# Kernel optimization log

Hardware: AMD Instinct MI355X
Metric: run time of the kernel (lower is better)

Reference implementation:

```python
import jax, jax.numpy as jnp
import numpy as np
import math

B, NRES, RPR = 1, 384, 3
L = NRES * RPR          # 1152 rigids
CS, CZ = 256, 128
CH, H, PQ, PV = 16, 8, 8, 12


def _ln(x, scale, bias):
    mu = jnp.mean(x, axis=-1, keepdims=True)
    var = jnp.var(x, axis=-1, keepdims=True)
    return (x - mu) * jax.lax.rsqrt(var + 1e-5) * scale + bias


def _quat_to_rot(q):
    q = q / jnp.linalg.norm(q, axis=-1, keepdims=True)
    w, x, y, z = q[..., 0], q[..., 1], q[..., 2], q[..., 3]
    r = jnp.stack([
        1 - 2 * (y * y + z * z), 2 * (x * y - w * z), 2 * (x * z + w * y),
        2 * (x * y + w * z), 1 - 2 * (x * x + z * z), 2 * (y * z - w * x),
        2 * (x * z - w * y), 2 * (y * z + w * x), 1 - 2 * (x * x + y * y),
    ], axis=-1)
    return r.reshape(q.shape[:-1] + (3, 3))


def setup_inputs() -> dict:
    key = jax.random.key(0)
    ks = jax.random.split(key, 20)
    s = jax.random.normal(ks[0], (B, L, CS), jnp.float32)
    z = jax.random.normal(ks[1], (B, NRES, NRES, CZ), jnp.float32)
    rot = _quat_to_rot(jax.random.normal(ks[2], (B, L, 4), jnp.float32))
    trans = 10.0 * jax.random.normal(ks[3], (B, L, 3), jnp.float32)
    mask = jnp.ones((B, L), jnp.float32)
    rigid_to_res_idx = jnp.broadcast_to(jnp.arange(L, dtype=jnp.int32) // RPR, (B, L))
    w = lambda k, sh: 0.02 * jax.random.normal(k, sh, jnp.float32)
    return {
        "s": s, "z": z, "rot": rot, "trans": trans, "mask": mask,
        "ln_s_scale": jnp.ones((CS,), jnp.float32), "ln_s_bias": jnp.zeros((CS,), jnp.float32),
        "ln_z_scale": jnp.ones((CZ,), jnp.float32), "ln_z_bias": jnp.zeros((CZ,), jnp.float32),
        "w_q": w(ks[4], (CS, H * CH)), "w_k": w(ks[5], (CS, H * CH)), "w_v": w(ks[6], (CS, H * CH)),
        "w_qp": w(ks[7], (CS, H * PQ * 3)), "w_kp": w(ks[8], (CS, H * PQ * 3)), "w_vp": w(ks[9], (CS, H * PV * 3)),
        "w_b": w(ks[10], (CZ, H)),
        "head_weights": jnp.full((H,), 0.5413, jnp.float32),  # softplus^-1(1)
        "w_out": w(ks[11], (H * (CH + CZ + PV * 4), CS)),
        "b_out": jnp.zeros((CS,), jnp.float32),
        "rigid_to_res_idx": rigid_to_res_idx,
    }


def reference(s, z, rot, trans, mask, ln_s_scale, ln_s_bias, ln_z_scale, ln_z_bias,
              w_q, w_k, w_v, w_qp, w_kp, w_vp, w_b, head_weights, w_out, b_out,
              rigid_to_res_idx):
    b_, l_ = s.shape[0], s.shape[1]
    idx = rigid_to_res_idx[0]                       # [L] rigid -> residue, shared over batch
    s_ln = _ln(s, ln_s_scale, ln_s_bias)            # [B,L,CS]
    z_ln = _ln(z, ln_z_scale, ln_z_bias)            # [B,N,N,CZ]

    q = (s_ln @ w_q).reshape(b_, l_, H, CH)
    k = (s_ln @ w_k).reshape(b_, l_, H, CH)
    v = (s_ln @ w_v).reshape(b_, l_, H, CH)

    # local points, then rigid-transform to global frame: x_g = R x + t
    q_p = (s_ln @ w_qp).reshape(b_, l_, H, PQ, 3)
    k_p = (s_ln @ w_kp).reshape(b_, l_, H, PQ, 3)
    v_p = (s_ln @ w_vp).reshape(b_, l_, H, PV, 3)
    t5 = trans[:, :, None, None, :]
    q_g = jnp.einsum("blij,blhpj->blhpi", rot, q_p) + t5
    k_g = jnp.einsum("blij,blhpj->blhpi", rot, k_p) + t5
    v_g = jnp.einsum("blij,blhpj->blhpi", rot, v_p) + t5

    # scalar qk term
    a = jnp.einsum("blhc,bjhc->bhlj", q, k) * math.sqrt(1.0 / (3 * CH))
    # pair bias, broadcast residue-pair -> rigid-pair
    b_res = z_ln @ w_b                                # [B,N,N,H]
    b_full = b_res[:, idx][:, :, idx]                 # [B,L,L,H]
    a = a + math.sqrt(1.0 / 3) * jnp.transpose(b_full, (0, 3, 1, 2))
    # point-distance term: ||q-k||^2 = |q|^2 + |k|^2 - 2 q.k (summed over P,3)
    hw = jax.nn.softplus(head_weights) * math.sqrt(1.0 / (3 * (PQ * 9.0 / 2)))
    qq = jnp.sum(q_g * q_g, axis=(-1, -2)).transpose(0, 2, 1)   # [B,H,L]
    kk = jnp.sum(k_g * k_g, axis=(-1, -2)).transpose(0, 2, 1)
    qk = jnp.einsum("blhpc,bjhpc->bhlj", q_g, k_g)
    d2 = qq[:, :, :, None] + kk[:, :, None, :] - 2.0 * qk
    a = a - 0.5 * d2 * hw[None, :, None, None]
    a = a + (mask[:, None, None, :] - 1.0) * 1e9
    attn = jax.nn.softmax(a, axis=-1)                 # [B,H,L,L]

    o = jnp.einsum("bhlj,bjhc->blhc", attn, v)        # [B,L,H,CH]
    o_pt_g = jnp.einsum("bhlj,bjhpc->blhpc", attn, v_g)
    # back to local frame of query rigid: R^T (x - t)
    o_pt = jnp.einsum("blji,blhpj->blhpi", rot, o_pt_g - t5)
    o_pt_norm = jnp.sqrt(jnp.sum(o_pt * o_pt, axis=-1) + 1e-8)  # [B,L,H,PV]
    # pair output: sum attention over rigids belonging to each key residue
    attn_res = attn.reshape(b_, H, l_, NRES, RPR).sum(-1)       # [B,H,L,N]
    z_l = z_ln[:, idx]                                           # [B,L,N,CZ]
    o_pair = jnp.einsum("bhln,blnc->blhc", attn_res, z_l)        # [B,L,H,CZ]

    cat = jnp.concatenate(
        [o, o_pt.reshape(b_, l_, H, PV * 3), o_pt_norm, o_pair], axis=-1
    ).reshape(b_, l_, H * (CH + PV * 4 + CZ))
    return cat @ w_out + b_out                        # [B,L,CS]
```

## Files before the change

kernel.cpp:

```cpp
#include <hip/hip_runtime.h>
#include <hip/hip_bf16.h>

#define L 1152
#define NRES 384
#define CS 256
#define CZ 128
#define H 8
#define CH 16
#define PQ 8
#define PV 12
#define PSTR 1088

#define OFF_SLN  0L
#define OFF_PROJ 294912L
#define OFF_WPK  1548288L
#define OFF_QCAT 1826816L
#define OFF_KCAT 2232320L
#define OFF_VCAT 2637824L
#define OFF_BRES 3227648L
#define OFF_MURS 4407296L
#define OFF_ATTN 4702208L
#define OFF_CAT  15319040L
#define OFF_PCAT 17088512L
#define OFF_RSTAT 18268160L
#define OFF_PAV  18286592L
#define OFF_POP  21825536L

__global__ __launch_bounds__(256) void k_ln_s(const float* s, const float* sc, const float* bi, float* sln){
  int l = blockIdx.x, t = threadIdx.x;
  __shared__ float red[CS];
  float x = s[(long)l*CS + t];
  red[t] = x; __syncthreads();
  for(int st=128; st>0; st>>=1){ if(t<st) red[t]+=red[t+st]; __syncthreads(); }
  float mu = red[0] * (1.f/CS); __syncthreads();
  float d = x - mu;
  red[t] = d*d; __syncthreads();
  for(int st=128; st>0; st>>=1){ if(t<st) red[t]+=red[t+st]; __syncthreads(); }
  float var = red[0]*(1.f/CS);
  sln[(long)l*CS + t] = d*rsqrtf(var + 1e-5f)*sc[t] + bi[t];
}

__global__ __launch_bounds__(256) void k_packw(const float* wq, const float* wk, const float* wv,
                        const float* wqp, const float* wkp, const float* wvp, float* wpack){
  int k = blockIdx.x, t = threadIdx.x;
  for(int c=t; c<PSTR; c+=256){
    float v;
    if(c<128)        v = wq [(long)k*128 + c];
    else if(c<256)   v = wk [(long)k*128 + c-128];
    else if(c<384)   v = wv [(long)k*128 + c-256];
    else if(c<576)   v = wqp[(long)k*192 + c-384];
    else if(c<768)   v = wkp[(long)k*192 + c-576];
    else if(c<1056)  v = wvp[(long)k*288 + c-768];
    else             v = 0.f;
    wpack[(long)k*PSTR + c] = v;
  }
}

__global__ __launch_bounds__(256) void k_proj(const float* sln, const float* wpack, float* proj){
  int l0 = blockIdx.x*64, c0 = blockIdx.y*64, t = threadIdx.x;
  __shared__ float a_s[32][68];
  __shared__ __align__(16) float w_s[32][68];
  int tr = t>>4, tc = t&15;
  float4 acc[4] = {{0,0,0,0},{0,0,0,0},{0,0,0,0},{0,0,0,0}};
  for(int kc=0; kc<8; kc++){
    int k0 = kc*32;
    {
      int row = t>>2, kk0 = (t&3)*8;
      const float4* src = (const float4*)(sln + (long)(l0+row)*256 + k0 + kk0);
      float4 v0 = src[0], v1 = src[1];
      a_s[kk0+0][row]=v0.x; a_s[kk0+1][row]=v0.y; a_s[kk0+2][row]=v0.z; a_s[kk0+3][row]=v0.w;
      a_s[kk0+4][row]=v1.x; a_s[kk0+5][row]=v1.y; a_s[kk0+6][row]=v1.z; a_s[kk0+7][row]=v1.w;
    }
    #pragma unroll
    for(int kk2=0; kk2<2; kk2++){
      int kk = (t>>4) + 16*kk2;
      *(float4*)&w_s[kk][(t&15)*4] = *(const float4*)(wpack + (long)(k0+kk)*PSTR + c0 + (t&15)*4);
    }
    __syncthreads();
    #pragma unroll 8
    for(int kk=0; kk<32; kk++){
      float4 a4 = *(const float4*)&a_s[kk][tr*4];
      float4 b4 = *(const float4*)&w_s[kk][tc*4];
      acc[0].x+=a4.x*b4.x; acc[0].y+=a4.x*b4.y; acc[0].z+=a4.x*b4.z; acc[0].w+=a4.x*b4.w;
      acc[1].x+=a4.y*b4.x; acc[1].y+=a4.y*b4.y; acc[1].z+=a4.y*b4.z; acc[1].w+=a4.y*b4.w;
      acc[2].x+=a4.z*b4.x; acc[2].y+=a4.z*b4.y; acc[2].z+=a4.z*b4.z; acc[2].w+=a4.z*b4.w;
      acc[3].x+=a4.w*b4.x; acc[3].y+=a4.w*b4.y; acc[3].z+=a4.w*b4.z; acc[3].w+=a4.w*b4.w;
    }
    __syncthreads();
  }
  #pragma unroll
  for(int r=0;r<4;r++)
    *(float4*)(proj + (long)(l0 + tr*4 + r)*PSTR + c0 + tc*4) = acc[r];
}

__global__ __launch_bounds__(256) void k_ln_z(const float* z, const float* sc, const float* bi,
                       const float* wb, float* murs, float* bres_t){
  int t = threadIdx.x;
  long rp0 = (long)blockIdx.x*32;
  int r = t>>3, part = t&7;
  long rp = rp0 + r;
  __shared__ __align__(16) float swb[8*132];
  __shared__ float SB[8][2];
  const float4* z4 = (const float4*)z;
  float4 x0 = z4[rp*32 + part*4 + 0];
  float4 x1 = z4[rp*32 + part*4 + 1];
  float4 x2 = z4[rp*32 + part*4 + 2];
  float4 x3 = z4[rp*32 + part*4 + 3];
  #pragma unroll
  for(int k2=0;k2<4;k2++){
    int e = t + k2*256; int h = e>>7, c = e&127;
    swb[h*132 + c] = sc[c]*wb[(long)c*8 + h];
  }
  __syncthreads();
  if(t < 64){
    int h = t>>3, seg = t&7;
    float S=0, Bv=0;
    #pragma unroll
    for(int i=0;i<16;i++){
      int c = seg*16+i;
      S  += swb[h*132+c];
      Bv += bi[c]*wb[(long)c*8 + h];
    }
    #pragma unroll
    for(int off=1;off<8;off<<=1){ S += __shfl_xor(S,off,64); Bv += __shfl_xor(Bv,off,64); }
    if(seg==0){ SB[h][0]=S; SB[h][1]=Bv; }
  }
  float s1 = x0.x+x0.y+x0.z+x0.w + x1.x+x1.y+x1.z+x1.w
           + x2.x+x2.y+x2.z+x2.w + x3.x+x3.y+x3.z+x3.w;
  float s2 = x0.x*x0.x+x0.y*x0.y+x0.z*x0.z+x0.w*x0.w
           + x1.x*x1.x+x1.y*x1.y+x1.z*x1.z+x1.w*x1.w
           + x2.x*x2.x+x2.y*x2.y+x2.z*x2.z+x2.w*x2.w
           + x3.x*x3.x+x3.y*x3.y+x3.z*x3.z+x3.w*x3.w;
  #pragma unroll
  for(int off=1;off<8;off<<=1){ s1 += __shfl_xor(s1,off,64); s2 += __shfl_xor(s2,off,64); }
  float mu = s1*(1.f/CZ);
  float var = s2*(1.f/CZ) - mu*mu;
  float rstd = rsqrtf(var + 1e-5f);
  if(part==0){ murs[rp*2]=mu; murs[rp*2+1]=rstd; }
  float acc[8];
  const float4* swb4 = (const float4*)swb;
  #pragma unroll
  for(int h=0;h<8;h++){
    float4 wa = swb4[h*33 + part*4 + 0];
    float4 wbv= swb4[h*33 + part*4 + 1];
    float4 wc = swb4[h*33 + part*4 + 2];
    float4 wd = swb4[h*33 + part*4 + 3];
    acc[h] = x0.x*wa.x + x0.y*wa.y + x0.z*wa.z + x0.w*wa.w
           + x1.x*wbv.x+ x1.y*wbv.y+ x1.z*wbv.z+ x1.w*wbv.w
           + x2.x*wc.x + x2.y*wc.y + x2.z*wc.z + x2.w*wc.w
           + x3.x*wd.x + x3.y*wd.y + x3.z*wd.z + x3.w*wd.w;
  }
  #pragma unroll
  for(int off=1;off<8;off<<=1){
    #pragma unroll
    for(int h=0;h<8;h++) acc[h] += __shfl_xor(acc[h],off,64);
  }
  __syncthreads();
  if(part==0){
    #pragma unroll
    for(int h=0;h<8;h++)
      bres_t[(long)h*147456 + rp] = rstd*(acc[h] - mu*SB[h][0]) + SB[h][1];
  }
}

__global__ __launch_bounds__(256) void k_rigid(const float* proj, const float* rot, const float* trans,
                        const float* mask, const float* hws,
                        float* qcat, float* kcat, float* vcat){
  int l = blockIdx.x, t = threadIdx.x;
  __shared__ float R[9], T[3], hwS[8], qgs[192], kgs[192];
  if(t<9) R[t]=rot[(long)l*9+t];
  if(t<3) T[t]=trans[(long)l*3+t];
  if(t>=16 && t<24) hwS[t-16] = log1pf(expf(hws[t-16]))*0.09622504486493764f;
  __syncthreads();
  const float* pr = proj + (long)l*PSTR;
  if(t<128){
    int h=t>>4, c=t&15;
    long base = ((long)h*L + l)*44;
    qcat[base + c] = 0.14433756729740643f * pr[t];
    kcat[base + c] = pr[128+t];
    vcat[((long)h*L + l)*64 + c] = pr[256+t];
  }
  if(t < 192){
    int h=t/24, m=t%24, p=m/3, i=m%3;
    float qa = R[i*3+0]*pr[384+h*24+p*3+0] + R[i*3+1]*pr[384+h*24+p*3+1]
             + R[i*3+2]*pr[384+h*24+p*3+2] + T[i];
    float ka = R[i*3+0]*pr[576+h*24+p*3+0] + R[i*3+1]*pr[576+h*24+p*3+1]
             + R[i*3+2]*pr[576+h*24+p*3+2] + T[i];
    qgs[t]=qa; kgs[t]=ka;
    long base = ((long)h*L + l)*44 + 16 + m;
    qcat[base] = hwS[h]*qa;
    kcat[base] = ka;
  }
  for(int it=t; it<288; it+=256){
    int h=it/36, m=it%36, p=m/3, i=m%3;
    float a = R[i*3+0]*pr[768+h*36+p*3+0] + R[i*3+1]*pr[768+h*36+p*3+1]
            + R[i*3+2]*pr[768+h*36+p*3+2] + T[i];
    vcat[((long)h*L + l)*64 + 16 + m] = a;
  }
  if(t < 96){
    int h=t/12, d=t%12;
    vcat[((long)h*L + l)*64 + 52 + d] = 0.f;
  }
  __syncthreads();
  if(t < 8){
    float qq=0, kk=0;
    #pragma unroll
    for(int m=0;m<24;m++){ qq += qgs[t*24+m]*qgs[t*24+m]; kk += kgs[t*24+m]*kgs[t*24+m]; }
    long base = ((long)t*L + l)*44;
    qcat[base + 40] = -0.5f*hwS[t]*qq;
    kcat[base + 40] = -0.5f*hwS[t]*kk + (mask[l]-1.f)*1e9f;
  }
}

__global__ __launch_bounds__(256) void k_scores(const float* qcat, const float* kcat,
                         const float* bres_t, const int* ridx, float* attn){
  int l0 = blockIdx.x*32, j0 = blockIdx.y*64, h = blockIdx.z;
  int t = threadIdx.x;
  __shared__ __align__(16) float q_s[32*44];
  __shared__ __align__(16) float k_s[64*44];
  __shared__ int rj_s[64];
  {
    const float* srcq = qcat + ((long)h*L + l0)*44;
    for(int i=t; i<32*44; i+=256) q_s[i]=srcq[i];
    const float* srck = kcat + ((long)h*L + j0)*44;
    for(int i=t; i<64*44; i+=256) k_s[i]=srck[i];
    if(t<64) rj_s[t]=ridx[j0+t];
  }
  __syncthreads();
  int a = t>>5;
  int b = t&31;
  float acc[4][2] = {{0,0},{0,0},{0,0},{0,0}};
  const float4* q4 = (const float4*)q_s;
  const float4* k4 = (const float4*)k_s;
  #pragma unroll
  for(int i=0;i<10;i++){
    float4 kA = k4[(long)b*11 + i];
    float4 kB = k4[(long)(b+32)*11 + i];
    #pragma unroll
    for(int r=0;r<4;r++){
      float4 qv = q4[(long)(a+8*r)*11 + i];
      acc[r][0] += qv.x*kA.x + qv.y*kA.y + qv.z*kA.z + qv.w*kA.w;
      acc[r][1] += qv.x*kB.x + qv.y*kB.y + qv.z*kB.z + qv.w*kB.w;
    }
  }
  float colc0 = k_s[b*44+40], colc1 = k_s[(b+32)*44+40];
  int rj0 = rj_s[b], rj1 = rj_s[b+32];
  const float* bbh = bres_t + (long)h*147456;
  #pragma unroll
  for(int r=0;r<4;r++){
    int row = a+8*r;
    float rowc = q_s[row*44+40];
    int rl = ridx[l0+row];
    const float* bb = bbh + (long)rl*NRES;
    float s0 = acc[r][0] + rowc + colc0 + 0.5773502691896258f*bb[rj0];
    float s1 = acc[r][1] + rowc + colc1 + 0.5773502691896258f*bb[rj1];
    float* arow = attn + ((long)h*L + l0+row)*L + j0;
    arow[b]    = s0;
    arow[b+32] = s1;
  }
}

__global__ __launch_bounds__(256) void k_rowstat(const float* attn, float* rowstat){
  long row = (long)blockIdx.x*4 + (threadIdx.x>>6);
  int lane = threadIdx.x & 63;
  const float* p = attn + row*L;
  float v[18];
  float m=-1e30f;
  #pragma unroll
  for(int i=0;i<18;i++){ v[i]=p[lane + i*64]; m=fmaxf(m,v[i]); }
  #pragma unroll
  for(int off=1;off<64;off<<=1) m=fmaxf(m,__shfl_xor(m,off,64));
  float s=0;
  #pragma unroll
  for(int i=0;i<18;i++) s+=__expf(v[i]-m);
  #pragma unroll
  for(int off=1;off<64;off<<=1) s+=__shfl_xor(s,off,64);
  if(lane==0){ rowstat[row*2]=m; rowstat[row*2+1]=1.f/s; }
}

__global__ __launch_bounds__(256) void k_av(const float* attn, const float* vcat,
                     const float* rowstat, float* pav){
  int lb = blockIdx.x, h = blockIdx.y, sp = blockIdx.z, t = threadIdx.x;
  int l0 = lb*32;
  __shared__ float a_s[64][33];
  __shared__ __align__(16) float v_s[64][68];
  int lgrp = t>>4, dgrp = t&15;
  float4 acc0 = {0,0,0,0}, acc1 = {0,0,0,0};
  const float* abase = attn + ((long)h*L + l0)*L;
  int al = t>>3, jj0 = (t&7)*8;
  float mrow = rowstat[((long)h*L + l0 + al)*2];
  float irow = rowstat[((long)h*L + l0 + al)*2 + 1];
  for(int jc=sp*3; jc<sp*3+3; jc++){
    int j0 = jc*64;
    {
      const float4* src = (const float4*)(abase + (long)al*L + j0 + jj0);
      float4 p0 = src[0], p1 = src[1];
      a_s[jj0+0][al]=__expf(p0.x-mrow)*irow;
      a_s[jj0+1][al]=__expf(p0.y-mrow)*irow;
      a_s[jj0+2][al]=__expf(p0.z-mrow)*irow;
      a_s[jj0+3][al]=__expf(p0.w-mrow)*irow;
      a_s[jj0+4][al]=__expf(p1.x-mrow)*irow;
      a_s[jj0+5][al]=__expf(p1.y-mrow)*irow;
      a_s[jj0+6][al]=__expf(p1.z-mrow)*irow;
      a_s[jj0+7][al]=__expf(p1.w-mrow)*irow;
    }
    {
      int jj = t>>2, seg = t&3;
      const float4* src = (const float4*)(vcat + ((long)h*L + j0 + jj)*64 + seg*16);
      float4 q0=src[0], q1=src[1], q2=src[2], q3=src[3];
      float4* dst = (float4*)&v_s[jj][seg*16];
      dst[0]=q0; dst[1]=q1; dst[2]=q2; dst[3]=q3;
    }
    __syncthreads();
    #pragma unroll 8
    for(int jj=0; jj<64; jj++){
      float a0 = a_s[jj][lgrp*2], a1 = a_s[jj][lgrp*2+1];
      const float4 vv = *(const float4*)&v_s[jj][dgrp*4];
      acc0.x+=a0*vv.x; acc0.y+=a0*vv.y; acc0.z+=a0*vv.z; acc0.w+=a0*vv.w;
      acc1.x+=a1*vv.x; acc1.y+=a1*vv.y; acc1.z+=a1*vv.z; acc1.w+=a1*vv.w;
    }
    __syncthreads();
  }
  float* dst = pav + (((long)sp*H + h)*L + l0 + lgrp*2)*64 + dgrp*4;
  *(float4*)dst = acc0;
  *(float4*)(dst + 64) = acc1;
}

__global__ __launch_bounds__(256) void k_avred(const float* pav, const float* rot, const float* trans,
                        float* cat){
  int lb = blockIdx.x, h = blockIdx.y, t = threadIdx.x;
  int l0 = lb*32;
  __shared__ __align__(16) float fin_s[32][64];
  #pragma unroll
  for(int k=0;k<2;k++){
    int fi = t + k*256;
    int l = fi>>4, c4 = fi&15;
    long base = (((long)h)*L + l0 + l)*64 + c4*4;
    float4 r = {0,0,0,0};
    #pragma unroll
    for(int p=0;p<6;p++){
      float4 a = *(const float4*)(pav + (long)p*589824 + base);
      r.x+=a.x; r.y+=a.y; r.z+=a.z; r.w+=a.w;
    }
    *(float4*)&fin_s[l][c4*4] = r;
  }
  __syncthreads();
  for(int it=t; it<32*16; it+=256){
    int l=it>>4, c=it&15;
    cat[(long)(l0+l)*1536 + h*192 + c] = fin_s[l][c];
  }
  for(int it=t; it<32*12; it+=256){
    int l=it/12, p=it%12;
    long gl = l0+l;
    float og0 = fin_s[l][16+p*3+0]-trans[gl*3+0];
    float og1 = fin_s[l][16+p*3+1]-trans[gl*3+1];
    float og2 = fin_s[l][16+p*3+2]-trans[gl*3+2];
    float* crow = cat + gl*1536 + h*192;
    float nrm=0;
    #pragma unroll
    for(int i=0;i<3;i++){
      float v = rot[gl*9+0+i]*og0 + rot[gl*9+3+i]*og1 + rot[gl*9+6+i]*og2;
      crow[16+p*3+i]=v; nrm+=v*v;
    }
    crow[52+p]=sqrtf(nrm+1e-8f);
  }
}

#define OPAIR_STEP(Z0,Z1,Z2,Z3,NB) { \
    float4 a0 = *(const float4*)&ar[0][th][NB]; \
    float4 a1 = *(const float4*)&ar[1][th][NB]; \
    float4 a2 = *(const float4*)&ar[2][th][NB]; \
    acc[0][0] += a0.x*Z0.x + a0.y*Z1.x + a0.z*Z2.x + a0.w*Z3.x; \
    acc[0][1] += a0.x*Z0.y + a0.y*Z1.y + a0.z*Z2.y + a0.w*Z3.y; \
    acc[0][2] += a0.x*Z0.z + a0.y*Z1.z + a0.z*Z2.z + a0.w*Z3.z; \
    acc[0][3] += a0.x*Z0.w + a0.y*Z1.w + a0.z*Z2.w + a0.w*Z3.w; \
    acc[1][0] += a1.x*Z0.x + a1.y*Z1.x + a1.z*Z2.x + a1.w*Z3.x; \
    acc[1][1] += a1.x*Z0.y + a1.y*Z1.y + a1.z*Z2.y + a1.w*Z3.y; \
    acc[1][2] += a1.x*Z0.z + a1.y*Z1.z + a1.z*Z2.z + a1.w*Z3.z; \
    acc[1][3] += a1.x*Z0.w + a1.y*Z1.w + a1.z*Z2.w + a1.w*Z3.w; \
    acc[2][0] += a2.x*Z0.x + a2.y*Z1.x + a2.z*Z2.x + a2.w*Z3.x; \
    acc[2][1] += a2.x*Z0.y + a2.y*Z1.y + a2.z*Z2.y + a2.w*Z3.y; \
    acc[2][2] += a2.x*Z0.z + a2.y*Z1.z + a2.z*Z2.z + a2.w*Z3.z; \
    acc[2][3] += a2.x*Z0.w + a2.y*Z1.w + a2.z*Z2.w + a2.w*Z3.w; }

__global__ __launch_bounds__(256) void k_opair(const float* attn, const float* z, const float* murs,
                        const float* rowstat,
                        const float* sc, const int* ridx, float* po){
  int r=blockIdx.x, sp=blockIdx.y, t=threadIdx.x;
  __shared__ __align__(16) float ar[3][H][96];
  __shared__ __align__(16) float mrs[96*2];
  __shared__ float rs_s[24][2];
  __shared__ float S1s[24];
  int rl = ridx[r*3];
  int n0 = sp*96;
  int tc = t&31, th = t>>5;
  const float* zbase = z + ((long)(rl*NRES + n0))*CZ + tc*4;
  float4 zc0 = *(const float4*)(zbase + 0L*CZ);
  float4 zc1 = *(const float4*)(zbase + 1L*CZ);
  float4 zc2 = *(const float4*)(zbase + 2L*CZ);
  float4 zc3 = *(const float4*)(zbase + 3L*CZ);
  if(t<24){
    int lo=t/8, h=t%8;
    long row = (long)h*L + r*3+lo;
    rs_s[t][0]=rowstat[row*2]; rs_s[t][1]=rowstat[row*2+1];
  }
  for(int i=t;i<192;i+=256) mrs[i]=murs[((long)rl*NRES + n0)*2 + i];
  __syncthreads();
  for(int it=t; it<3*H*96; it+=256){
    int lo = it/(H*96);
    int rem = it - lo*(H*96);
    int h = rem/96, n = rem - h*96;
    const float* arow = attn + ((long)h*L + r*3+lo)*L + (n0+n)*3;
    float m = rs_s[lo*8+h][0], iv = rs_s[lo*8+h][1];
    ar[lo][h][n]=(__expf(arow[0]-m)+__expf(arow[1]-m)+__expf(arow[2]-m))*iv*mrs[n*2+1];
  }
  __syncthreads();
  if(t<192){
    int row=t>>3, seg=t&7;
    const float* arr = ((const float*)ar) + row*96 + seg*12;
    const float* mur = mrs + seg*24;
    float s1=0;
    #pragma unroll
    for(int q2=0;q2<12;q2++) s1 += arr[q2]*mur[q2*2];
    s1 += __shfl_xor(s1,1,64); s1 += __shfl_xor(s1,2,64); s1 += __shfl_xor(s1,4,64);
    if(seg==0) S1s[row]=s1;
  }
  __syncthreads();
  float acc[3][4]={};
  for(int nb=0; nb<88; nb+=8){
    float4 zn0 = *(const float4*)(zbase + (long)(nb+4)*CZ);
    float4 zn1 = *(const float4*)(zbase + (long)(nb+5)*CZ);
    float4 zn2 = *(const float4*)(zbase + (long)(nb+6)*CZ);
    float4 zn3 = *(const float4*)(zbase + (long)(nb+7)*CZ);
    OPAIR_STEP(zc0,zc1,zc2,zc3, nb);
    zc0 = *(const float4*)(zbase + (long)(nb+ 8)*CZ);
    zc1 = *(const float4*)(zbase + (long)(nb+ 9)*CZ);
    zc2 = *(const float4*)(zbase + (long)(nb+10)*CZ);
    zc3 = *(const float4*)(zbase + (long)(nb+11)*CZ);
    OPAIR_STEP(zn0,zn1,zn2,zn3, nb+4);
  }
  {
    float4 zn0 = *(const float4*)(zbase + 92L*CZ);
    float4 zn1 = *(const float4*)(zbase + 93L*CZ);
    float4 zn2 = *(const float4*)(zbase + 94L*CZ);
    float4 zn3 = *(const float4*)(zbase + 95L*CZ);
    OPAIR_STEP(zc0,zc1,zc2,zc3, 88);
    OPAIR_STEP(zn0,zn1,zn2,zn3, 92);
  }
  float4 sc4 = *(const float4*)(sc + tc*4);
  #pragma unroll
  for(int lo=0;lo<3;lo++){
    float s1v = S1s[lo*8+th];
    float4 o = { sc4.x*(acc[lo][0]-s1v), sc4.y*(acc[lo][1]-s1v),
                 sc4.z*(acc[lo][2]-s1v), sc4.w*(acc[lo][3]-s1v) };
    *(float4*)(po + ((long)sp*L + (long)(r*3+lo))*1024 + th*128 + tc*4) = o;
  }
}

__global__ __launch_bounds__(256) void k_opred(const float* po, const float* bi, float* cat){
  int i = blockIdx.x*256 + threadIdx.x;
  const float4* p = (const float4*)po;
  float4 a = p[i], b = p[i + 294912], c = p[i + 589824], d = p[i + 884736];
  int l = i>>8, rem = i&255;
  int h = rem>>5, c4 = rem&31;
  float4 bv = ((const float4*)bi)[c4];
  float4 r = {a.x+b.x+c.x+d.x+bv.x, a.y+b.y+c.y+d.y+bv.y,
              a.z+b.z+c.z+d.z+bv.z, a.w+b.w+c.w+d.w+bv.w};
  ((float4*)cat)[(long)l*384 + h*48 + 16 + c4] = r;
}

__global__ __launch_bounds__(256) void k_final(const float* cat, const float* wout, float* pcat){
  int l0 = blockIdx.x*32, c0 = blockIdx.y*32, kp = blockIdx.z, t = threadIdx.x;
  __shared__ float a_s[64][33];
  __shared__ __align__(16) float w_s[64][36];
  int tr = t>>3, tc = t&7;
  float4 acc = {0,0,0,0};
  for(int kc=0; kc<6; kc++){
    int k0 = kp*384 + kc*64;
    {
      int row = t>>3, kk0 = (t&7)*8;
      const float4* src = (const float4*)(cat + (long)(l0+row)*1536 + k0 + kk0);
      float4 v0 = src[0], v1 = src[1];
      a_s[kk0+0][row]=v0.x; a_s[kk0+1][row]=v0.y; a_s[kk0+2][row]=v0.z; a_s[kk0+3][row]=v0.w;
      a_s[kk0+4][row]=v1.x; a_s[kk0+5][row]=v1.y; a_s[kk0+6][row]=v1.z; a_s[kk0+7][row]=v1.w;
    }
    #pragma unroll
    for(int kk2=0; kk2<2; kk2++){
      int kk = (t>>3) + 32*kk2;
      *(float4*)&w_s[kk][(t&7)*4] = *(const float4*)(wout + (long)(k0+kk)*256 + c0 + (t&7)*4);
    }
    __syncthreads();
    #pragma unroll 8
    for(int kk=0; kk<64; kk++){
      float a0 = a_s[kk][tr];
      float4 b4 = *(const float4*)&w_s[kk][tc*4];
      acc.x+=a0*b4.x; acc.y+=a0*b4.y; acc.z+=a0*b4.z; acc.w+=a0*b4.w;
    }
    __syncthreads();
  }
  *(float4*)(pcat + ((long)kp*L + l0+tr)*256 + c0 + tc*4) = acc;
}

__global__ __launch_bounds__(256) void k_redout(const float* pcat, const float* bout, float* out){
  int i = blockIdx.x*256 + threadIdx.x;
  const float4* p = (const float4*)pcat;
  float4 a = p[i], b = p[i+73728], c = p[i+147456], d = p[i+221184];
  float4 bv = ((const float4*)bout)[i&63];
  float4 r;
  r.x = a.x+b.x+c.x+d.x+bv.x;
  r.y = a.y+b.y+c.y+d.y+bv.y;
  r.z = a.z+b.z+c.z+d.z+bv.z;
  r.w = a.w+b.w+c.w+d.w+bv.w;
  ((float4*)out)[i] = r;
}

extern "C" void kernel_launch(void* const* d_in, const int* in_sizes, int n_in,
                              void* d_out, int out_size, void* d_ws, size_t ws_size,
                              hipStream_t stream) {
  const float* s      = (const float*)d_in[0];
  const float* z      = (const float*)d_in[1];
  const float* rot    = (const float*)d_in[2];
  const float* trans  = (const float*)d_in[3];
  const float* mask   = (const float*)d_in[4];
  const float* lnss   = (const float*)d_in[5];
  const float* lnsb   = (const float*)d_in[6];
  const float* lnzs   = (const float*)d_in[7];
  const float* lnzb   = (const float*)d_in[8];
  const float* wq     = (const float*)d_in[9];
  const float* wk     = (const float*)d_in[10];
  const float* wv     = (const float*)d_in[11];
  const float* wqp    = (const float*)d_in[12];
  const float* wkp    = (const float*)d_in[13];
  const float* wvp    = (const float*)d_in[14];
  const float* wb     = (const float*)d_in[15];
  const float* hws    = (const float*)d_in[16];
  const float* wout   = (const float*)d_in[17];
  const float* bout   = (const float*)d_in[18];
  const int*  ridx    = (const int*)d_in[19];

  float* ws  = (float*)d_ws;
  float* out = (float*)d_out;

  float* sln  = ws + OFF_SLN;
  float* proj = ws + OFF_PROJ;
  float* wpk  = ws + OFF_WPK;
  float* qcat = ws + OFF_QCAT;
  float* kcat = ws + OFF_KCAT;
  float* vcat = ws + OFF_VCAT;
  float* bres = ws + OFF_BRES;
  float* murs = ws + OFF_MURS;
  float* attn = ws + OFF_ATTN;
  float* cat  = ws + OFF_CAT;
  float* pcat = ws + OFF_PCAT;
  float* rstat= ws + OFF_RSTAT;
  float* pav  = ws + OFF_PAV;
  float* po   = ws + OFF_POP;

  k_packw<<<dim3(256), dim3(256), 0, stream>>>(wq, wk, wv, wqp, wkp, wvp, wpk);
  k_ln_s<<<dim3(L), dim3(CS), 0, stream>>>(s, lnss, lnsb, sln);
  k_proj<<<dim3(18,17), dim3(256), 0, stream>>>(sln, wpk, proj);
  k_ln_z<<<dim3(NRES*NRES/32), dim3(256), 0, stream>>>(z, lnzs, lnzb, wb, murs, bres);
  k_rigid<<<dim3(L), dim3(256), 0, stream>>>(proj, rot, trans, mask, hws, qcat, kcat, vcat);
  k_scores<<<dim3(L/32, L/64, H), dim3(256), 0, stream>>>(qcat, kcat, bres, ridx, attn);
  k_rowstat<<<dim3(H*L/4), dim3(256), 0, stream>>>(attn, rstat);
  k_av<<<dim3(L/32, H, 6), dim3(256), 0, stream>>>(attn, vcat, rstat, pav);
  k_avred<<<dim3(L/32, H), dim3(256), 0, stream>>>(pav, rot, trans, cat);
  k_opair<<<dim3(NRES, 4), dim3(256), 0, stream>>>(attn, z, murs, rstat, lnzs, ridx, po);
  k_opred<<<dim3(1152), dim3(256), 0, stream>>>(po, lnzb, cat);
  k_final<<<dim3(36,8,4), dim3(256), 0, stream>>>(cat, wout, pcat);
  k_redout<<<dim3(288), dim3(256), 0, stream>>>(pcat, bout, out);
}
```

Before: 323.9 us.

## Compute per-residue attention sums in k_av and reuse them in k_opair

```diff
diff --git a/kernel.cpp b/kernel.cpp
--- a/kernel.cpp
+++ b/kernel.cpp
@@ -25,6 +25,7 @@
 #define OFF_RSTAT 18268160L
 #define OFF_PAV  18286592L
 #define OFF_POP  21825536L
+#define OFF_ARES 26544128L
 
 __global__ __launch_bounds__(256) void k_ln_s(const float* s, const float* sc, const float* bi, float* sln){
   int l = blockIdx.x, t = threadIdx.x;
@@ -279,30 +280,47 @@
 }
 
 __global__ __launch_bounds__(256) void k_av(const float* attn, const float* vcat,
-                     const float* rowstat, float* pav){
+                     const float* rowstat, float* pav, float* ares){
   int lb = blockIdx.x, h = blockIdx.y, sp = blockIdx.z, t = threadIdx.x;
   int l0 = lb*32;
   __shared__ float a_s[64][33];
   __shared__ __align__(16) float v_s[64][68];
+  __shared__ float ares_s[32][64];
   int lgrp = t>>4, dgrp = t&15;
   float4 acc0 = {0,0,0,0}, acc1 = {0,0,0,0};
   const float* abase = attn + ((long)h*L + l0)*L;
   int al = t>>3, jj0 = (t&7)*8;
   float mrow = rowstat[((long)h*L + l0 + al)*2];
   float irow = rowstat[((long)h*L + l0 + al)*2 + 1];
-  for(int jc=sp*3; jc<sp*3+3; jc++){
-    int j0 = jc*64;
+  for(int i=t;i<32*64;i+=256) ((float*)ares_s)[i]=0.f;
+  __syncthreads();
+  for(int jcl=0; jcl<3; jcl++){
+    int j0 = (sp*3+jcl)*64;
     {
       const float4* src = (const float4*)(abase + (long)al*L + j0 + jj0);
       float4 p0 = src[0], p1 = src[1];
-      a_s[jj0+0][al]=__expf(p0.x-mrow)*irow;
-      a_s[jj0+1][al]=__expf(p0.y-mrow)*irow;
-      a_s[jj0+2][al]=__expf(p0.z-mrow)*irow;
-      a_s[jj0+3][al]=__expf(p0.w-mrow)*irow;
-      a_s[jj0+4][al]=__expf(p1.x-mrow)*irow;
-      a_s[jj0+5][al]=__expf(p1.y-mrow)*irow;
-      a_s[jj0+6][al]=__expf(p1.z-mrow)*irow;
-      a_s[jj0+7][al]=__expf(p1.w-mrow)*irow;
+      float e0=__expf(p0.x-mrow)*irow, e1=__expf(p0.y-mrow)*irow;
+      float e2=__expf(p0.z-mrow)*irow, e3=__expf(p0.w-mrow)*irow;
+      float e4=__expf(p1.x-mrow)*irow, e5=__expf(p1.y-mrow)*irow;
+      float e6=__expf(p1.z-mrow)*irow, e7=__expf(p1.w-mrow)*irow;
+      a_s[jj0+0][al]=e0; a_s[jj0+1][al]=e1; a_s[jj0+2][al]=e2; a_s[jj0+3][al]=e3;
+      a_s[jj0+4][al]=e4; a_s[jj0+5][al]=e5; a_s[jj0+6][al]=e6; a_s[jj0+7][al]=e7;
+      int jb = jcl*64 + jj0;
+      int tb = jb/3, r3 = jb - tb*3;
+      if(r3==0){
+        atomicAdd(&ares_s[al][tb  ], e0+e1+e2);
+        atomicAdd(&ares_s[al][tb+1], e3+e4+e5);
+        atomicAdd(&ares_s[al][tb+2], e6+e7);
+      } else if(r3==1){
+        atomicAdd(&ares_s[al][tb  ], e0+e1);
+        atomicAdd(&ares_s[al][tb+1], e2+e3+e4);
+        atomicAdd(&ares_s[al][tb+2], e5+e6+e7);
+      } else {
+        atomicAdd(&ares_s[al][tb  ], e0);
+        atomicAdd(&ares_s[al][tb+1], e1+e2+e3);
+        atomicAdd(&ares_s[al][tb+2], e4+e5+e6);
+        atomicAdd(&ares_s[al][tb+3], e7);
+      }
     }
     {
       int jj = t>>2, seg = t&3;
@@ -324,6 +342,10 @@
   float* dst = pav + (((long)sp*H + h)*L + l0 + lgrp*2)*64 + dgrp*4;
   *(float4*)dst = acc0;
   *(float4*)(dst + 64) = acc1;
+  for(int i=t;i<2048;i+=256){
+    int l=i>>6, n=i&63;
+    ares[((long)h*L + l0+l)*NRES + sp*64 + n] = ares_s[l][n];
+  }
 }
 
 __global__ __launch_bounds__(256) void k_avred(const float* pav, const float* rot, const float* trans,
@@ -383,13 +405,11 @@
     acc[2][2] += a2.x*Z0.z + a2.y*Z1.z + a2.z*Z2.z + a2.w*Z3.z; \
     acc[2][3] += a2.x*Z0.w + a2.y*Z1.w + a2.z*Z2.w + a2.w*Z3.w; }
 
-__global__ __launch_bounds__(256) void k_opair(const float* attn, const float* z, const float* murs,
-                        const float* rowstat,
+__global__ __launch_bounds__(256) void k_opair(const float* ares, const float* z, const float* murs,
                         const float* sc, const int* ridx, float* po){
   int r=blockIdx.x, sp=blockIdx.y, t=threadIdx.x;
   __shared__ __align__(16) float ar[3][H][96];
   __shared__ __align__(16) float mrs[96*2];
-  __shared__ float rs_s[24][2];
   __shared__ float S1s[24];
   int rl = ridx[r*3];
   int n0 = sp*96;
@@ -399,20 +419,13 @@
   float4 zc1 = *(const float4*)(zbase + 1L*CZ);
   float4 zc2 = *(const float4*)(zbase + 2L*CZ);
   float4 zc3 = *(const float4*)(zbase + 3L*CZ);
-  if(t<24){
-    int lo=t/8, h=t%8;
-    long row = (long)h*L + r*3+lo;
-    rs_s[t][0]=rowstat[row*2]; rs_s[t][1]=rowstat[row*2+1];
-  }
   for(int i=t;i<192;i+=256) mrs[i]=murs[((long)rl*NRES + n0)*2 + i];
   __syncthreads();
   for(int it=t; it<3*H*96; it+=256){
     int lo = it/(H*96);
     int rem = it - lo*(H*96);
     int h = rem/96, n = rem - h*96;
-    const float* arow = attn + ((long)h*L + r*3+lo)*L + (n0+n)*3;
-    float m = rs_s[lo*8+h][0], iv = rs_s[lo*8+h][1];
-    ar[lo][h][n]=(__expf(arow[0]-m)+__expf(arow[1]-m)+__expf(arow[2]-m))*iv*mrs[n*2+1];
+    ar[lo][h][n] = ares[((long)h*L + r*3+lo)*NRES + n0 + n] * mrs[n*2+1];
   }
   __syncthreads();
   if(t<192){
@@ -555,6 +568,7 @@
   float* rstat= ws + OFF_RSTAT;
   float* pav  = ws + OFF_PAV;
   float* po   = ws + OFF_POP;
+  float* ares = ws + OFF_ARES;
 
   k_packw<<<dim3(256), dim3(256), 0, stream>>>(wq, wk, wv, wqp, wkp, wvp, wpk);
   k_ln_s<<<dim3(L), dim3(CS), 0, stream>>>(s, lnss, lnsb, sln);
@@ -563,9 +577,9 @@
   k_rigid<<<dim3(L), dim3(256), 0, stream>>>(proj, rot, trans, mask, hws, qcat, kcat, vcat);
   k_scores<<<dim3(L/32, L/64, H), dim3(256), 0, stream>>>(qcat, kcat, bres, ridx, attn);
   k_rowstat<<<dim3(H*L/4), dim3(256), 0, stream>>>(attn, rstat);
-  k_av<<<dim3(L/32, H, 6), dim3(256), 0, stream>>>(attn, vcat, rstat, pav);
+  k_av<<<dim3(L/32, H, 6), dim3(256), 0, stream>>>(attn, vcat, rstat, pav, ares);
   k_avred<<<dim3(L/32, H), dim3(256), 0, stream>>>(pav, rot, trans, cat);
-  k_opair<<<dim3(NRES, 4), dim3(256), 0, stream>>>(attn, z, murs, rstat, lnzs, ridx, po);
+  k_opair<<<dim3(NRES, 4), dim3(256), 0, stream>>>(ares, z, murs, lnzs, ridx, po);
   k_opred<<<dim3(1152), dim3(256), 0, stream>>>(po, lnzb, cat);
   k_final<<<dim3(36,8,4), dim3(256), 0, stream>>>(cat, wout, pcat);
   k_redout<<<dim3(288), dim3(256), 0, stream>>>(pcat, bout, out);
```

Result: slower. 343.2 us (+6.0%).
